# Kernel tuning notes

Hardware: AMD Instinct MI355X
Metric: run time of the kernel (lower is better)

## Reference

```python
import jax, jax.numpy as jnp
import numpy as np

B, S, D, H, KP, DK = 4, 2048, 1024, 16, 8, 3
DD = D // H
NEG = -1.0e9


def dense(x, W, b):
    return x @ W + b


def dw_conv_causal(x, w, b):
    # x: [B,S,D], w: [DK,D] per-channel kernel, b: [D]; left pad DK-1 zeros -> VALID conv
    xp = jnp.pad(x, ((0, 0), (DK - 1, 0), (0, 0)))
    y = b
    for t in range(DK):
        y = y + xp[:, t:t + S, :] * w[t]
    return y


def split_heads(x):
    return x.reshape(B, S, H, DD).transpose(0, 2, 1, 3)  # [B,H,S,DD]


def pool_causal(x):
    # left pad KP-1 zeros along seq, avg_pool window=stride=KP, VALID
    xp = jnp.pad(x, ((0, 0), (0, 0), (KP - 1, 0), (0, 0)))
    n = (S - 1) // KP + 1  # TF VALID output length
    return xp[:, :, :n * KP, :].reshape(B, H, n, KP, DD).mean(axis=3)


def forward(q, k, v, Wq, bq, Wk, bk, Wv, bv, Wup, bup, Wc, bc,
            wcq, bcq, wck, bck, wcv, bcv):
    norm = float(DD) ** -0.25
    qh = dense(q, Wq, bq) * norm
    kh = dense(k, Wk, bk) * norm
    vh = dense(v, Wv, bv)
    q_in = split_heads(dw_conv_causal(qh, wcq, bcq))
    k_in = split_heads(dw_conv_causal(kh, wck, bck))
    v_in = split_heads(dw_conv_causal(vh, wcv, bcv))
    qp = pool_causal(q_in)  # [B,H,n,DD]
    kp = pool_causal(k_in)
    vp = pool_causal(v_in)
    n = qp.shape[2]
    mask = NEG * (1.0 - jnp.tril(jnp.ones((n, n), dtype=qp.dtype)))
    logits = jnp.einsum('bhnd,bhmd->bhnm', qp, kp) + mask
    attn = jax.nn.softmax(logits, axis=-1)
    out = jnp.einsum('bhnm,bhmd->bhnd', attn, vp)  # [B,H,n,DD]
    up = jnp.repeat(out, KP, axis=2)[:, :, :S, :]  # upsample + crop
    up = dense(up, Wup, bup)
    merged = up.transpose(0, 2, 1, 3).reshape(B, S, D)
    return dense(merged, Wc, bc)


def setup_inputs() -> dict:
    key = jax.random.key(0)
    ks = jax.random.split(key, 20)
    w = lambda i, shp: jax.random.normal(ks[i], shp, dtype=jnp.float32) * 0.02
    return {
        'q': jax.random.normal(ks[0], (B, S, D), dtype=jnp.float32),
        'k': jax.random.normal(ks[1], (B, S, D), dtype=jnp.float32),
        'v': jax.random.normal(ks[2], (B, S, D), dtype=jnp.float32),
        'Wq': w(3, (D, D)), 'bq': jnp.zeros((D,), jnp.float32),
        'Wk': w(4, (D, D)), 'bk': jnp.zeros((D,), jnp.float32),
        'Wv': w(5, (D, D)), 'bv': jnp.zeros((D,), jnp.float32),
        'Wup': w(6, (DD, DD)), 'bup': jnp.zeros((DD,), jnp.float32),
        'Wc': w(7, (D, D)), 'bc': jnp.zeros((D,), jnp.float32),
        'wcq': w(8, (DK, D)), 'bcq': jnp.zeros((D,), jnp.float32),
        'wck': w(9, (DK, D)), 'bck': jnp.zeros((D,), jnp.float32),
        'wcv': w(10, (DK, D)), 'bcv': jnp.zeros((D,), jnp.float32),
    }


def reference(q, k, v, Wq, bq, Wk, bk, Wv, bv, Wup, bup, Wc, bc,
              wcq, bcq, wck, bck, wcv, bcv):
    return forward(q, k, v, Wq, bq, Wk, bk, Wv, bv, Wup, bup, Wc, bc,
                   wcq, bcq, wck, bck, wcv, bcv)
```

## Files before the change

### kernel.cpp

```cpp
#include <hip/hip_runtime.h>
#include <cstdint>
#include <cstddef>

#define Bc  4
#define Sc  2048
#define Dc  1024
#define Hc  16
#define DDc 64
#define Nc  256

typedef unsigned short u16;
typedef unsigned int   u32;
typedef __bf16 bf16_t;
typedef bf16_t bf16x8 __attribute__((ext_vector_type(8)));
typedef float  f32x4  __attribute__((ext_vector_type(4)));

__device__ __forceinline__ u16 f2bf(float x) {
    u32 u = __float_as_uint(x);
    return (u16)((u + 0x7FFFu + ((u >> 16) & 1u)) >> 16);
}
__device__ __forceinline__ u32 pack2(float a, float b) {
    return (u32)f2bf(a) | ((u32)f2bf(b) << 16);
}
__device__ __forceinline__ uint2 pack4v(f32x4 x) {
    return make_uint2(pack2(x[0], x[1]), pack2(x[2], x[3]));
}
__device__ __forceinline__ float bf2f(u16 x) {
    return __uint_as_float((u32)x << 16);
}

__device__ __forceinline__ void gload_lds16(const void* gp, void* lp) {
    __builtin_amdgcn_global_load_lds(
        reinterpret_cast<const __attribute__((address_space(1))) void*>(
            reinterpret_cast<uintptr_t>(gp)),
        reinterpret_cast<__attribute__((address_space(3))) void*>(
            reinterpret_cast<uintptr_t>(lp)),
        16, 0, 0);
}

__device__ __forceinline__ void stage64(const char* src, size_t kb, u16* lds,
                                        int lane, size_t rstride) {
    const int rowoff = lane >> 3;
    const int srcg   = ((lane & 7) ^ (rowoff & 7)) * 16;
    const char* s0 = src + kb + (size_t)srcg;
    #pragma unroll
    for (int i = 0; i < 8; ++i)
        gload_lds16(s0 + (size_t)(8 * i + rowoff) * rstride,
                    (char*)lds + i * 1024);
}

__device__ __forceinline__ void frag_read(const u16* lds, int mi, int quad,
                                          bf16x8 f[4][2]) {
    const int key = mi & 7;
    #pragma unroll
    for (int i = 0; i < 4; ++i)
        #pragma unroll
        for (int kc = 0; kc < 2; ++kc) {
            int g = (kc * 4 + quad) ^ key;
            f[i][kc] = *(const bf16x8*)(lds + (i * 16 + mi) * 64 + g * 8);
        }
}

__global__ __launch_bounds__(256) void prep_stage(
    const float* __restrict__ q,  const float* __restrict__ k,  const float* __restrict__ v,
    const float* __restrict__ Wq, const float* __restrict__ Wk,
    const float* __restrict__ Wv, const float* __restrict__ Wc,
    const float* __restrict__ Wup,
    const float* __restrict__ wcq, const float* __restrict__ wck, const float* __restrict__ wcv,
    const float* __restrict__ bcq, const float* __restrict__ bck, const float* __restrict__ bcv,
    const float* __restrict__ bq,  const float* __restrict__ bk,  const float* __restrict__ bv,
    u16* __restrict__ Wt3, u16* __restrict__ Wtc, float* __restrict__ biasT,
    u16* __restrict__ WupT, u16* __restrict__ A3)
{
    __shared__ __align__(16) float LS[10 * 1024];
    float (*T)[65] = (float(*)[65])LS;
    const int bid = blockIdx.x;
    const int tid = threadIdx.x;

    if (bid < 1024) {
        const int z = bid >> 8;
        const float* W = (z == 0) ? Wq : (z == 1) ? Wk : (z == 2) ? Wv : Wc;
        const int k0 = ((bid >> 4) & 15) * 64, n0 = (bid & 15) * 64;
        const int c = tid & 63, r4 = tid >> 6;
        #pragma unroll
        for (int i = 0; i < 16; ++i) {
            int r = i * 4 + r4;
            T[r][c] = W[(size_t)(k0 + r) * 1024 + n0 + c];
        }
        __syncthreads();
        if (z < 3) {
            const float* wc = (z == 0) ? wcq : (z == 1) ? wck : wcv;
            const float fs = 0.125f * ((z == 2) ? 1.0f : 0.35355339059327373f);
            u16* dst0 = Wt3 + (size_t)z * 3145728;
            #pragma unroll
            for (int i = 0; i < 16; ++i) {
                int r = i * 4 + r4;
                int n = n0 + r;
                float w0 = wc[n], w1 = wc[1024 + n], w2 = wc[2048 + n];
                float s2 = fs * w2, s1 = s2 + fs * w1, s0 = s1 + fs * w0;
                float x = T[c][r];
                u16* dst = dst0 + (size_t)n * 3072 + k0 + c;
                dst[0]    = f2bf(x * s0);
                dst[1024] = f2bf(x * s1);
                dst[2048] = f2bf(x * s2);
            }
        } else {
            #pragma unroll
            for (int i = 0; i < 16; ++i) {
                int r = i * 4 + r4;
                Wtc[(size_t)(n0 + r) * 1024 + k0 + c] = f2bf(T[c][r]);
            }
        }
        return;
    }

    if (bid < 1036) {
        int gid = (bid - 1024) * 256 + tid;
        int c = gid & 1023, z = gid >> 10;
        const float* wc    = (z == 0) ? wcq : (z == 1) ? wck : wcv;
        const float* bconv = (z == 0) ? bcq : (z == 1) ? bck : bcv;
        const float* bl    = (z == 0) ? bq  : (z == 1) ? bk  : bv;
        const float nrm = (z == 2) ? 1.0f : 0.35355339059327373f;
        float w0 = wc[c], w1 = wc[1024 + c], w2 = wc[2048 + c];
        float bc_ = bconv[c], bl_ = bl[c];
        float* dst = biasT + (size_t)z * 3072 + c;
        dst[0]    = 0.125f * (bc_ + nrm * bl_ * w2);
        dst[1024] = 0.125f * (8.f * bc_ + nrm * bl_ * (7.f * w0 + 8.f * w1 + 8.f * w2));
        dst[2048] = 0.125f * (8.f * bc_ + nrm * bl_ * 8.f * (w0 + w1 + w2));
        return;
    }

    if (bid == 1036) {
        const int c = tid & 63, r4 = tid >> 6;
        #pragma unroll
        for (int i = 0; i < 16; ++i) {
            int r = i * 4 + r4;
            T[r][c] = Wup[r * 64 + c];
        }
        __syncthreads();
        #pragma unroll
        for (int i = 0; i < 16; ++i) {
            int r = i * 4 + r4;
            WupT[r * 64 + c] = f2bf(T[c][r]);
        }
        return;
    }

    int sbid0 = bid - 1037;
    int sbid  = (sbid0 & 7) * 384 + (sbid0 >> 3);
    int t = sbid & 255, b = (sbid >> 8) & 3, inp = sbid >> 10;
    const float* src = (inp == 0) ? q : (inp == 1) ? k : v;
    const char* base = (const char*)(src + (size_t)b * Sc * Dc);
    const int tid16 = tid * 16;
    const int wvoff = (tid & 192) * 16;
    char* LSB = (char*)LS;

    const int nneg = (t >= 2) ? 0 : (t == 1 ? 1 : 9);
    const f32x4 zz = (f32x4){0.f, 0.f, 0.f, 0.f};
    for (int i = 0; i < nneg; ++i)
        *(f32x4*)(LSB + i * 4096 + tid16) = zz;
    #pragma unroll
    for (int i = 0; i < 10; ++i)
        if (i >= nneg)
            gload_lds16(base + (size_t)(8 * t - 9 + i) * 4096 + tid16,
                        LSB + i * 4096 + wvoff);
    __syncthreads();

    f32x4 rr[10];
    #pragma unroll
    for (int i = 0; i < 10; ++i)
        rr[i] = *(const f32x4*)(LSB + i * 4096 + tid16);

    f32x4 A0 = ((rr[0] + rr[1]) + (rr[2] + rr[3])) + ((rr[4] + rr[5]) + (rr[6] + rr[7]));
    f32x4 B1 = rr[8] - rr[0];
    f32x4 B2 = rr[9] - rr[1];

    size_t s0 = (size_t)inp * 3145728 + (size_t)(b * 256 + t) * 3072 + tid * 4;
    *(uint2*)(A3 + s0)        = pack4v(A0);
    *(uint2*)(A3 + s0 + 1024) = pack4v(B1);
    *(uint2*)(A3 + s0 + 2048) = pack4v(B2);
}

__global__ __launch_bounds__(64) void gemm_qkv(
    const u16* __restrict__ A3, const u16* __restrict__ Wt3,
    const float* __restrict__ biasT,
    u16* __restrict__ qb, u16* __restrict__ kb, u16* __restrict__ vt)
{
    __shared__ __align__(16) u16 S[2][2][4096];

    const int lane = threadIdx.x;
    const int bid = blockIdx.x;

    if (bid >= 768) {
        const int vb = bid - 768;
        #pragma unroll
        for (int bh4 = 0; bh4 < 4; ++bh4) {
            const int bh = vb * 4 + bh4;
            #pragma unroll
            for (int it = 0; it < 8; ++it) {
                int gidx = it * 64 + lane;
                int row  = 64 + (gidx >> 5);
                int c0   = (gidx & 31) * 8;
                u32 fill = (row == 64) ? 0x3F803F80u : 0u;
                *(uint4*)(vt + (size_t)bh * 20480 + (size_t)row * 256 + c0) =
                    make_uint4(fill, fill, fill, fill);
            }
        }
        return;
    }

    const int mi   = lane & 15;
    const int quad = lane >> 4;

    const int wg  = (bid & 7) * 96 + (bid >> 3);
    const int z   = wg >> 8;
    const int m0  = ((wg >> 4) & 15) * 64;
    const int n0  = (wg & 15) * 64;

    const char* Ab = (const char*)(A3  + (size_t)z * 3145728) + (size_t)m0 * 6144;
    const char* Bb = (const char*)(Wt3 + (size_t)z * 3145728) + (size_t)n0 * 6144;

    f32x4 acc[4][4];
    #pragma unroll
    for (int i = 0; i < 4; ++i)
        #pragma unroll
        for (int j = 0; j < 4; ++j)
            acc[i][j] = (f32x4){0.f, 0.f, 0.f, 0.f};

    stage64(Ab, 0, S[0][0], lane, 6144);
    stage64(Bb, 0, S[0][1], lane, 6144);

    #pragma unroll 1
    for (int t = 0; t < 48; ++t) {
        const int cur = t & 1;
        if (t < 47) {
            stage64(Ab, (size_t)(t + 1) * 128, S[cur ^ 1][0], lane, 6144);
            stage64(Bb, (size_t)(t + 1) * 128, S[cur ^ 1][1], lane, 6144);
            asm volatile("s_waitcnt vmcnt(16)" ::: "memory");
        } else {
            asm volatile("s_waitcnt vmcnt(0)" ::: "memory");
        }
        __builtin_amdgcn_sched_barrier(0);

        bf16x8 af[4][2], bf[4][2];
        frag_read(S[cur][0], mi, quad, af);
        frag_read(S[cur][1], mi, quad, bf);

        #pragma unroll
        for (int kc = 0; kc < 2; ++kc)
            #pragma unroll
            for (int i = 0; i < 4; ++i)
                #pragma unroll
                for (int j = 0; j < 4; ++j)
                    acc[i][j] = __builtin_amdgcn_mfma_f32_16x16x32_bf16(af[i][kc], bf[j][kc], acc[i][j], 0, 0, 0);
    }

    const float* bT = biasT + (size_t)z * 3072;
    if (z == 2) {
        #pragma unroll
        for (int j = 0; j < 4; ++j) {
            const int col = n0 + j * 16 + mi;
            const int h = col >> 6, d = col & 63;
            #pragma unroll
            for (int i = 0; i < 4; ++i) {
                const int row = m0 + i * 16 + quad * 4;
                const int b = row >> 8, t0 = row & 255;
                const int bh = b * 16 + h;
                u16 w[4];
                #pragma unroll
                for (int r = 0; r < 4; ++r) {
                    int t = t0 + r;
                    w[r] = f2bf(acc[i][j][r] + bT[(t < 2 ? t : 2) * 1024 + col]);
                }
                *(uint2*)(vt + (size_t)bh * 20480 + (size_t)d * 256 + t0) =
                    make_uint2((u32)w[0] | ((u32)w[1] << 16), (u32)w[2] | ((u32)w[3] << 16));
            }
        }
    } else {
        u16* dst = z ? kb : qb;
        #pragma unroll
        for (int j = 0; j < 4; ++j) {
            const int col = n0 + j * 16 + mi;
            const int h = col >> 6, d = col & 63;
            #pragma unroll
            for (int i = 0; i < 4; ++i) {
                const int row = m0 + i * 16 + quad * 4;
                const int b = row >> 8;
                const int bh = b * 16 + h;
                #pragma unroll
                for (int r = 0; r < 4; ++r) {
                    int t = (row & 255) + r;
                    dst[(((size_t)bh * 256 + t) << 6) + d] =
                        f2bf(acc[i][j][r] + bT[(t < 2 ? t : 2) * 1024 + col]);
                }
            }
        }
    }
}

__global__ __launch_bounds__(64) void attn_mfma(
    const u16* __restrict__ qb, const u16* __restrict__ kb,
    const u16* __restrict__ vt, const u16* __restrict__ WupT,
    const float* __restrict__ bup, u16* __restrict__ ms)
{
    __shared__ __align__(16) u16 P[64 * 72];
    const int qt   = blockIdx.x;
    const int bh   = blockIdx.y;
    const int lane = threadIdx.x;
    const int mi   = lane & 15;
    const int quad = lane >> 4;

    const u16* Qb = qb + (((size_t)bh * 256 + qt * 64) << 6);
    const u16* Kb = kb + ((size_t)bh << 14);
    const u16* Vt = vt + (size_t)bh * 80 * 256;

    bf16x8 qf[4][2];
    #pragma unroll
    for (int it = 0; it < 4; ++it)
        #pragma unroll
        for (int kc = 0; kc < 2; ++kc)
            qf[it][kc] = *(const bf16x8*)(Qb + ((it * 16 + mi) << 6) + kc * 32 + quad * 8);

    f32x4 o[4][5];
    #pragma unroll
    for (int it = 0; it < 4; ++it)
        #pragma unroll
        for (int jn = 0; jn < 5; ++jn)
            o[it][jn] = (f32x4){0.f, 0.f, 0.f, 0.f};

    for (int kt = 0; kt <= qt; ++kt) {
        bf16x8 kf[4][2];
        #pragma unroll
        for (int jt = 0; jt < 4; ++jt)
            #pragma unroll
            for (int kc = 0; kc < 2; ++kc)
                kf[jt][kc] = *(const bf16x8*)(Kb + ((kt * 64 + jt * 16 + mi) << 6) + kc * 32 + quad * 8);

        f32x4 s[4][4];
        #pragma unroll
        for (int it = 0; it < 4; ++it)
            #pragma unroll
            for (int jt = 0; jt < 4; ++jt)
                s[it][jt] = (f32x4){0.f, 0.f, 0.f, 0.f};
        #pragma unroll
        for (int kc = 0; kc < 2; ++kc)
            #pragma unroll
            for (int it = 0; it < 4; ++it)
                #pragma unroll
                for (int jt = 0; jt < 4; ++jt)
                    s[it][jt] = __builtin_amdgcn_mfma_f32_16x16x32_bf16(qf[it][kc], kf[jt][kc], s[it][jt], 0, 0, 0);

        const bool diag = (kt == qt);
        #pragma unroll
        for (int it = 0; it < 4; ++it)
            #pragma unroll
            for (int jt = 0; jt < 4; ++jt)
                #pragma unroll
                for (int r = 0; r < 4; ++r) {
                    int qrow = it * 16 + quad * 4 + r;
                    int kcol = jt * 16 + mi;
                    float e = __expf(s[it][jt][r]);
                    if (diag && kcol > qrow) e = 0.f;
                    P[qrow * 72 + kcol] = f2bf(e);
                }

        bf16x8 pf[4][2];
        #pragma unroll
        for (int it = 0; it < 4; ++it)
            #pragma unroll
            for (int kc = 0; kc < 2; ++kc)
                pf[it][kc] = *(const bf16x8*)(P + (it * 16 + mi) * 72 + kc * 32 + quad * 8);

        bf16x8 vf[5][2];
        #pragma unroll
        for (int jn = 0; jn < 5; ++jn)
            #pragma unroll
            for (int kc = 0; kc < 2; ++kc)
                vf[jn][kc] = *(const bf16x8*)(Vt + (size_t)(jn * 16 + mi) * 256 + kt * 64 + kc * 32 + quad * 8);

        #pragma unroll
        for (int kc = 0; kc < 2; ++kc)
            #pragma unroll
            for (int it = 0; it < 4; ++it)
                #pragma unroll
                for (int jn = 0; jn < 5; ++jn)
                    o[it][jn] = __builtin_amdgcn_mfma_f32_16x16x32_bf16(pf[it][kc], vf[jn][kc], o[it][jn], 0, 0, 0);
    }

    #pragma unroll
    for (int it = 0; it < 4; ++it) {
        float inv[4];
        #pragma unroll
        for (int r = 0; r < 4; ++r) {
            float lv = __shfl(o[it][4][r], (lane & 48));
            inv[r] = 1.0f / lv;
        }
        #pragma unroll
        for (int jn = 0; jn < 4; ++jn)
            #pragma unroll
            for (int r = 0; r < 4; ++r) {
                int row = it * 16 + quad * 4 + r;
                P[row * 72 + jn * 16 + mi] = f2bf(o[it][jn][r] * inv[r]);
            }
    }

    bf16x8 ga[4][2], wf[4][2];
    #pragma unroll
    for (int it = 0; it < 4; ++it)
        #pragma unroll
        for (int kc = 0; kc < 2; ++kc)
            ga[it][kc] = *(const bf16x8*)(P + (it * 16 + mi) * 72 + kc * 32 + quad * 8);
    #pragma unroll
    for (int jn = 0; jn < 4; ++jn)
        #pragma unroll
        for (int kc = 0; kc < 2; ++kc)
            wf[jn][kc] = *(const bf16x8*)(WupT + (jn * 16 + mi) * 64 + kc * 32 + quad * 8);

    f32x4 u[4][4];
    #pragma unroll
    for (int it = 0; it < 4; ++it)
        #pragma unroll
        for (int jn = 0; jn < 4; ++jn)
            u[it][jn] = (f32x4){0.f, 0.f, 0.f, 0.f};
    #pragma unroll
    for (int kc = 0; kc < 2; ++kc)
        #pragma unroll
        for (int it = 0; it < 4; ++it)
            #pragma unroll
            for (int jn = 0; jn < 4; ++jn)
                u[it][jn] = __builtin_amdgcn_mfma_f32_16x16x32_bf16(ga[it][kc], wf[jn][kc], u[it][jn], 0, 0, 0);

    const int b = bh >> 4, h = bh & 15;
    #pragma unroll
    for (int jn = 0; jn < 4; ++jn) {
        const int dp = jn * 16 + mi;
        const float bv = bup[dp];
        #pragma unroll
        for (int it = 0; it < 4; ++it)
            #pragma unroll
            for (int r = 0; r < 4; ++r) {
                int m = qt * 64 + it * 16 + quad * 4 + r;
                ms[((size_t)(b * 256 + m) << 10) + h * 64 + dp] = f2bf(u[it][jn][r] + bv);
            }
    }
}

__global__ __launch_bounds__(64) void gemm_out_up(
    const u16* __restrict__ A, const u16* __restrict__ Bt,
    const float* __restrict__ bias, float* __restrict__ out)
{
    __shared__ __align__(16) u16 S[2][2][4096];
    __shared__ __align__(16) float Cs[64][68];

    const int lane = threadIdx.x;
    const int mi   = lane & 15;
    const int quad = lane >> 4;

    const int bid = blockIdx.x;
    const int wg  = (bid & 7) * 32 + (bid >> 3);
    const int m0  = (wg >> 4) * 64;
    const int n0  = (wg & 15) * 64;

    const char* Ab = (const char*)A  + (size_t)m0 * 2048;
    const char* Bb = (const char*)Bt + (size_t)n0 * 2048;

    f32x4 acc[4][4];
    #pragma unroll
    for (int i = 0; i < 4; ++i)
        #pragma unroll
        for (int j = 0; j < 4; ++j)
            acc[i][j] = (f32x4){0.f, 0.f, 0.f, 0.f};

    stage64(Ab, 0, S[0][0], lane, 2048);
    stage64(Bb, 0, S[0][1], lane, 2048);

    #pragma unroll 1
    for (int t = 0; t < 16; ++t) {
        const int cur = t & 1;
        if (t < 15) {
            stage64(Ab, (size_t)(t + 1) * 128, S[cur ^ 1][0], lane, 2048);
            stage64(Bb, (size_t)(t + 1) * 128, S[cur ^ 1][1], lane, 2048);
            asm volatile("s_waitcnt vmcnt(16)" ::: "memory");
        } else {
            asm volatile("s_waitcnt vmcnt(0)" ::: "memory");
        }
        __builtin_amdgcn_sched_barrier(0);

        bf16x8 af[4][2], bf[4][2];
        frag_read(S[cur][0], mi, quad, af);
        frag_read(S[cur][1], mi, quad, bf);

        #pragma unroll
        for (int kc = 0; kc < 2; ++kc)
            #pragma unroll
            for (int i = 0; i < 4; ++i)
                #pragma unroll
                for (int j = 0; j < 4; ++j)
                    acc[i][j] = __builtin_amdgcn_mfma_f32_16x16x32_bf16(af[i][kc], bf[j][kc], acc[i][j], 0, 0, 0);
    }

    #pragma unroll
    for (int j = 0; j < 4; ++j) {
        const float bv = bias[n0 + j * 16 + mi];
        #pragma unroll
        for (int i = 0; i < 4; ++i)
            #pragma unroll
            for (int r = 0; r < 4; ++r)
                Cs[i * 16 + quad * 4 + r][j * 16 + mi] = acc[i][j][r] + bv;
    }

    const int col4 = lane & 15;
    #pragma unroll 4
    for (int it = 0; it < 128; ++it) {
        const int crow = it >> 1;
        const int rep  = ((it & 1) << 2) + (lane >> 4);
        float4 val = *(const float4*)&Cs[crow][col4 * 4];
        const int R = m0 + crow;
        const int b = R >> 8, tc = R & 255;
        float* po = out + (((size_t)((b << 11) + (tc << 3) + rep)) << 10) + n0 + (col4 << 2);
        *(float4*)po = val;
    }
}

extern "C" void kernel_launch(void* const* d_in, const int* in_sizes, int n_in,
                              void* d_out, int out_size, void* d_ws, size_t ws_size,
                              hipStream_t stream) {
    const float* q   = (const float*)d_in[0];
    const float* k   = (const float*)d_in[1];
    const float* v   = (const float*)d_in[2];
    const float* Wq  = (const float*)d_in[3];
    const float* bq  = (const float*)d_in[4];
    const float* Wk  = (const float*)d_in[5];
    const float* bk  = (const float*)d_in[6];
    const float* Wv  = (const float*)d_in[7];
    const float* bv  = (const float*)d_in[8];
    const float* Wup = (const float*)d_in[9];
    const float* bup = (const float*)d_in[10];
    const float* Wc  = (const float*)d_in[11];
    const float* bc  = (const float*)d_in[12];
    const float* wcq = (const float*)d_in[13];
    const float* bcq = (const float*)d_in[14];
    const float* wck = (const float*)d_in[15];
    const float* bck = (const float*)d_in[16];
    const float* wcv = (const float*)d_in[17];
    const float* bcv = (const float*)d_in[18];

    u16* A3 = (u16*)d_out;

    char* wsb = (char*)d_ws;
    u16*   Wt3   = (u16*)wsb;
    u16*   Wtc   = (u16*)(wsb + 18874368);
    float* biasT = (float*)(wsb + 20971520);
    u16*   qb    = (u16*)(wsb + 21008384);
    u16*   kb    = (u16*)(wsb + 23105536);
    u16*   vt    = (u16*)(wsb + 25202688);
    u16*   WupT  = (u16*)(wsb + 27824128);
    u16*   ms    = (u16*)(wsb + 32018432);

    prep_stage<<<4109, 256, 0, stream>>>(q, k, v, Wq, Wk, Wv, Wc, Wup,
                                         wcq, wck, wcv, bcq, bck, bcv,
                                         bq, bk, bv, Wt3, Wtc, biasT, WupT, A3);
    gemm_qkv<<<784, 64, 0, stream>>>(A3, Wt3, biasT, qb, kb, vt);
    attn_mfma<<<dim3(4, 64), 64, 0, stream>>>(qb, kb, vt, WupT, bup, ms);
    gemm_out_up<<<256, 64, 0, stream>>>(ms, Wtc, bc, (float*)d_out);
}
```

Measured before the change: 241.0 us.

## Split input staging into sliding-window ring-buffer kernel separate from weight prep

Moves the per-pooled-window input staging out of the combined prep kernel into its own kernel. Each block now walks 8 consecutive pooled windows and keeps an 18-row LDS ring buffer, so the 2 rows shared between neighbouring windows are loaded once and loads for the next window overlap compute through explicit vmcnt waits. The weight transposes move to a separate kernel. This cuts redundant global reads of q/k/v and per-block overhead, but adds one launch and gives the staging kernel far fewer blocks (384), which may leave the GPU underused.

```diff
diff --git a/kernel.cpp b/kernel.cpp
--- a/kernel.cpp
+++ b/kernel.cpp
@@ -61,8 +61,7 @@
         }
 }
 
-__global__ __launch_bounds__(256) void prep_stage(
-    const float* __restrict__ q,  const float* __restrict__ k,  const float* __restrict__ v,
+__global__ __launch_bounds__(256) void prep_misc(
     const float* __restrict__ Wq, const float* __restrict__ Wk,
     const float* __restrict__ Wv, const float* __restrict__ Wc,
     const float* __restrict__ Wup,
@@ -70,10 +69,9 @@
     const float* __restrict__ bcq, const float* __restrict__ bck, const float* __restrict__ bcv,
     const float* __restrict__ bq,  const float* __restrict__ bk,  const float* __restrict__ bv,
     u16* __restrict__ Wt3, u16* __restrict__ Wtc, float* __restrict__ biasT,
-    u16* __restrict__ WupT, u16* __restrict__ A3)
+    u16* __restrict__ WupT)
 {
-    __shared__ __align__(16) float LS[10 * 1024];
-    float (*T)[65] = (float(*)[65])LS;
+    __shared__ float T[64][65];
     const int bid = blockIdx.x;
     const int tid = threadIdx.x;
 
@@ -130,55 +128,93 @@
         return;
     }
 
-    if (bid == 1036) {
-        const int c = tid & 63, r4 = tid >> 6;
-        #pragma unroll
-        for (int i = 0; i < 16; ++i) {
-            int r = i * 4 + r4;
-            T[r][c] = Wup[r * 64 + c];
-        }
-        __syncthreads();
-        #pragma unroll
-        for (int i = 0; i < 16; ++i) {
-            int r = i * 4 + r4;
-            WupT[r * 64 + c] = f2bf(T[c][r]);
-        }
-        return;
-    }
-
-    int sbid0 = bid - 1037;
-    int sbid  = (sbid0 & 7) * 384 + (sbid0 >> 3);
-    int t = sbid & 255, b = (sbid >> 8) & 3, inp = sbid >> 10;
+    const int c = tid & 63, r4 = tid >> 6;
+    #pragma unroll
+    for (int i = 0; i < 16; ++i) {
+        int r = i * 4 + r4;
+        T[r][c] = Wup[r * 64 + c];
+    }
+    __syncthreads();
+    #pragma unroll
+    for (int i = 0; i < 16; ++i) {
+        int r = i * 4 + r4;
+        WupT[r * 64 + c] = f2bf(T[c][r]);
+    }
+}
+
+__global__ __launch_bounds__(256) void stage_slide(
+    const float* __restrict__ q, const float* __restrict__ k,
+    const float* __restrict__ v, u16* __restrict__ A3)
+{
+    __shared__ __align__(16) float RING[18 * 1024];
+    const int tid  = threadIdx.x;
+    const int bid0 = blockIdx.x;
+    const int bid  = (bid0 & 7) * 48 + (bid0 >> 3);
+    const int ck   = bid & 31;
+    const int b    = (bid >> 5) & 3;
+    const int inp  = bid >> 7;
+    const int t0   = ck * 8;
+
     const float* src = (inp == 0) ? q : (inp == 1) ? k : v;
     const char* base = (const char*)(src + (size_t)b * Sc * Dc);
     const int tid16 = tid * 16;
     const int wvoff = (tid & 192) * 16;
-    char* LSB = (char*)LS;
-
-    const int nneg = (t >= 2) ? 0 : (t == 1 ? 1 : 9);
-    const f32x4 zz = (f32x4){0.f, 0.f, 0.f, 0.f};
-    for (int i = 0; i < nneg; ++i)
-        *(f32x4*)(LSB + i * 4096 + tid16) = zz;
-    #pragma unroll
-    for (int i = 0; i < 10; ++i)
-        if (i >= nneg)
-            gload_lds16(base + (size_t)(8 * t - 9 + i) * 4096 + tid16,
-                        LSB + i * 4096 + wvoff);
-    __syncthreads();
-
-    f32x4 rr[10];
-    #pragma unroll
-    for (int i = 0; i < 10; ++i)
-        rr[i] = *(const f32x4*)(LSB + i * 4096 + tid16);
-
-    f32x4 A0 = ((rr[0] + rr[1]) + (rr[2] + rr[3])) + ((rr[4] + rr[5]) + (rr[6] + rr[7]));
-    f32x4 B1 = rr[8] - rr[0];
-    f32x4 B2 = rr[9] - rr[1];
-
-    size_t s0 = (size_t)inp * 3145728 + (size_t)(b * 256 + t) * 3072 + tid * 4;
-    *(uint2*)(A3 + s0)        = pack4v(A0);
-    *(uint2*)(A3 + s0 + 1024) = pack4v(B1);
-    *(uint2*)(A3 + s0 + 2048) = pack4v(B2);
+    char* RB = (char*)RING;
+
+    if (t0 == 0) {
+        const f32x4 zz = (f32x4){0.f, 0.f, 0.f, 0.f};
+        #pragma unroll
+        for (int i = 0; i < 9; ++i)
+            *(f32x4*)(RB + (9 + i) * 4096 + tid16) = zz;
+        gload_lds16(base + tid16, RB + wvoff);
+    } else {
+        const int r = 8 * t0 - 9;
+        const int s = r % 18;
+        #pragma unroll
+        for (int i = 0; i < 10; ++i) {
+            int si = s + i; if (si >= 18) si -= 18;
+            gload_lds16(base + (size_t)(r + i) * 4096 + tid16, RB + si * 4096 + wvoff);
+        }
+    }
+
+    int s0 = (8 * t0 - 9) % 18; if (s0 < 0) s0 += 18;
+
+    #pragma unroll 1
+    for (int st = 0; st < 8; ++st) {
+        const int t = t0 + st;
+        if (st < 7) {
+            const int rn = 8 * t + 1;
+            int sn = s0 + 10; if (sn >= 18) sn -= 18;
+            #pragma unroll
+            for (int i = 0; i < 8; ++i) {
+                int si = sn + i; if (si >= 18) si -= 18;
+                gload_lds16(base + (size_t)(rn + i) * 4096 + tid16,
+                            RB + si * 4096 + wvoff);
+            }
+            if (st == 0) asm volatile("s_waitcnt vmcnt(8)" ::: "memory");
+            else         asm volatile("s_waitcnt vmcnt(11)" ::: "memory");
+        } else {
+            asm volatile("s_waitcnt vmcnt(3)" ::: "memory");
+        }
+        __builtin_amdgcn_sched_barrier(0);
+
+        f32x4 rr[10];
+        #pragma unroll
+        for (int i = 0; i < 10; ++i) {
+            int si = s0 + i; if (si >= 18) si -= 18;
+            rr[i] = *(const f32x4*)(RB + si * 4096 + tid16);
+        }
+        f32x4 A0 = ((rr[0] + rr[1]) + (rr[2] + rr[3])) + ((rr[4] + rr[5]) + (rr[6] + rr[7]));
+        f32x4 B1 = rr[8] - rr[0];
+        f32x4 B2 = rr[9] - rr[1];
+
+        size_t so = (size_t)inp * 3145728 + (size_t)(b * 256 + t) * 3072 + tid * 4;
+        *(uint2*)(A3 + so)        = pack4v(A0);
+        *(uint2*)(A3 + so + 1024) = pack4v(B1);
+        *(uint2*)(A3 + so + 2048) = pack4v(B2);
+
+        s0 += 8; if (s0 >= 18) s0 -= 18;
+    }
 }
 
 __global__ __launch_bounds__(64) void gemm_qkv(
@@ -557,9 +593,10 @@
     u16*   WupT  = (u16*)(wsb + 27824128);
     u16*   ms    = (u16*)(wsb + 32018432);
 
-    prep_stage<<<4109, 256, 0, stream>>>(q, k, v, Wq, Wk, Wv, Wc, Wup,
-                                         wcq, wck, wcv, bcq, bck, bcv,
-                                         bq, bk, bv, Wt3, Wtc, biasT, WupT, A3);
+    prep_misc<<<1037, 256, 0, stream>>>(Wq, Wk, Wv, Wc, Wup,
+                                        wcq, wck, wcv, bcq, bck, bcv,
+                                        bq, bk, bv, Wt3, Wtc, biasT, WupT);
+    stage_slide<<<384, 256, 0, stream>>>(q, k, v, A3);
     gemm_qkv<<<784, 64, 0, stream>>>(A3, Wt3, biasT, qb, kb, vt);
     attn_mfma<<<dim3(4, 64), 64, 0, stream>>>(qb, kb, vt, WupT, bup, ms);
     gemm_out_up<<<256, 64, 0, stream>>>(ms, Wtc, bc, (float*)d_out);
```

Result: no change. 243.8 us (+1.2%).
